# Kernel tuning notes

Measured on AMD Instinct MI355X. Metric: run time of the kernel, lower is better.

The kernel has to match this reference:

```python
import jax, jax.numpy as jnp
import numpy as np

N_NODES = 50000
N_PAIRS = 625000
F = 128

def setup_inputs() -> dict:
    key = jax.random.key(0)
    k1, k2, k3, k4, k5 = jax.random.split(key, 5)
    x = jax.random.normal(k1, (N_NODES, F), dtype=jnp.float32)
    alpha_ij = jax.random.normal(k2, (N_PAIRS,), dtype=jnp.float32)
    idx_i = jax.random.randint(k3, (N_PAIRS,), 0, N_NODES, dtype=jnp.int32)
    idx_j = jax.random.randint(k4, (N_PAIRS,), 0, N_NODES, dtype=jnp.int32)
    # Dense(F, use_bias=False) kernel, shape (F_in, F_out)
    W = jax.random.normal(k5, (F, F), dtype=jnp.float32) / np.sqrt(F)
    return {"x": x, "alpha_ij": alpha_ij, "idx_i": idx_i, "idx_j": idx_j, "W": W}

def reference(x, alpha_ij, idx_i, idx_j, W):
    # dense projection on nodes (n,F) @ (F,F) -> (n,F)
    v = jnp.matmul(x, W)
    # gather neighbor values, scale by attention coeff: (n_pairs, F)
    msg = alpha_ij[:, None] * v[idx_j]
    # scatter-sum back to center atoms
    return jax.ops.segment_sum(msg, segment_ids=idx_i, num_segments=x.shape[0])
```

## Files before the change

### kernel.cpp

```cpp
#include <hip/hip_runtime.h>
#include <stdint.h>

#define FDIM 128
#define BR 64
#define NB_C 196
#define QC 4096
#define PPB 2048

typedef short  s8v   __attribute__((ext_vector_type(8)));
typedef float  f4v   __attribute__((ext_vector_type(4)));
typedef unsigned short u8v __attribute__((ext_vector_type(8)));

__device__ __forceinline__ unsigned short f2bf(float f) {
    union { float f; uint32_t u; } c; c.f = f;
    uint32_t u = c.u;
    return (unsigned short)((u + 0x7fffu + ((u >> 16) & 1u)) >> 16);
}
__device__ __forceinline__ float bflo2f(uint32_t g) {
    union { uint32_t u; float f; } c; c.u = g << 16; return c.f;
}
__device__ __forceinline__ float bfhi2f(uint32_t g) {
    union { uint32_t u; float f; } c; c.u = g & 0xffff0000u; return c.f;
}

__global__ __launch_bounds__(256) void prep(const float* __restrict__ W,
                                            unsigned short* __restrict__ Wt,
                                            int* __restrict__ gcur) {
    int i = blockIdx.x * 256 + threadIdx.x;
    if (i < FDIM * FDIM) {
        int n = i & 127, k = i >> 7;
        Wt[n * FDIM + k] = f2bf(W[k * FDIM + n]);
    }
    if (i < NB_C) gcur[i] = 0;
}

__global__ __launch_bounds__(256) void fused_gemm_pass1(
        const float* __restrict__ x,
        const unsigned short* __restrict__ Wt,
        unsigned short* __restrict__ v,
        const int* __restrict__ idx_i,
        const int* __restrict__ idx_j,
        const float* __restrict__ alpha,
        int* __restrict__ gcur,
        unsigned long long* __restrict__ qrec,
        int n_rows, int n_pairs, int PB) {
    __shared__ unsigned short As[BR][FDIM + 8];

    if ((int)blockIdx.x < PB) {
        __shared__ int hist[NB_C];
        __shared__ int base_s[NB_C];
        const int t = threadIdx.x;
        const int start = blockIdx.x * PPB;

        if (t < NB_C) hist[t] = 0;
        __syncthreads();

        unsigned long long rec[8];
        int bkt[8];
#pragma unroll
        for (int i = 0; i < 8; ++i) {
            int p = start + t + i * 256;
            bkt[i] = -1;
            if (p < n_pairs) {
                int ii = idx_i[p];
                int b  = ii >> 8;
                bkt[i] = b;
                rec[i] = (unsigned long long)(uint32_t)(idx_j[p] | ((ii & 255) << 16))
                       | ((unsigned long long)(uint32_t)__float_as_int(alpha[p]) << 32);
                atomicAdd(&hist[b], 1);
            }
        }
        __syncthreads();
        if (t < NB_C) {
            int h = hist[t];
            base_s[t] = (h > 0) ? atomicAdd(&gcur[t], h) : 0;
            hist[t] = 0;
        }
        __syncthreads();
#pragma unroll
        for (int i = 0; i < 8; ++i) {
            int b = bkt[i];
            if (b >= 0) {
                int lp  = atomicAdd(&hist[b], 1);
                int pos = base_s[b] + lp;
                if (pos < QC)
                    qrec[(size_t)b * QC + pos] = rec[i];
            }
        }
        return;
    }

    const int t = threadIdx.x;
    const int row0 = (blockIdx.x - PB) * BR;
    {
        int r  = t >> 2;
        int c0 = (t & 3) * 32;
        int grow = row0 + r;
        const float* src = x + (size_t)grow * FDIM + c0;
#pragma unroll
        for (int it = 0; it < 4; ++it) {
            float4 xa = make_float4(0.f, 0.f, 0.f, 0.f);
            float4 xb = make_float4(0.f, 0.f, 0.f, 0.f);
            if (grow < n_rows) {
                xa = *(const float4*)(src + it * 8);
                xb = *(const float4*)(src + it * 8 + 4);
            }
            u8v pk;
            pk[0] = f2bf(xa.x); pk[1] = f2bf(xa.y); pk[2] = f2bf(xa.z); pk[3] = f2bf(xa.w);
            pk[4] = f2bf(xb.x); pk[5] = f2bf(xb.y); pk[6] = f2bf(xb.z); pk[7] = f2bf(xb.w);
            *(u8v*)(&As[r][c0 + it * 8]) = pk;
        }
    }
    __syncthreads();

    const int w    = t >> 6;
    const int lane = t & 63;
    const int rt   = (w & 1) * 32;
    const int ct   = (w >> 1) * 64;
    const int lrow = lane & 15;
    const int kq   = (lane >> 4) * 8;

    f4v acc[2][4];
#pragma unroll
    for (int i = 0; i < 2; ++i)
#pragma unroll
        for (int j = 0; j < 4; ++j)
            acc[i][j] = (f4v){0.f, 0.f, 0.f, 0.f};

#pragma unroll
    for (int ks = 0; ks < 4; ++ks) {
        const int k0 = ks * 32 + kq;
        const unsigned short* wb = Wt + (size_t)(ct + lrow) * FDIM + k0;
        s8v b0 = *(const s8v*)(wb);
        s8v b1 = *(const s8v*)(wb + 16 * FDIM);
        s8v b2 = *(const s8v*)(wb + 32 * FDIM);
        s8v b3 = *(const s8v*)(wb + 48 * FDIM);
        s8v a0 = *(const s8v*)(&As[rt + lrow][k0]);
        s8v a1 = *(const s8v*)(&As[rt + 16 + lrow][k0]);
        acc[0][0] = __builtin_amdgcn_mfma_f32_16x16x32_bf16(a0, b0, acc[0][0], 0, 0, 0);
        acc[0][1] = __builtin_amdgcn_mfma_f32_16x16x32_bf16(a0, b1, acc[0][1], 0, 0, 0);
        acc[0][2] = __builtin_amdgcn_mfma_f32_16x16x32_bf16(a0, b2, acc[0][2], 0, 0, 0);
        acc[0][3] = __builtin_amdgcn_mfma_f32_16x16x32_bf16(a0, b3, acc[0][3], 0, 0, 0);
        acc[1][0] = __builtin_amdgcn_mfma_f32_16x16x32_bf16(a1, b0, acc[1][0], 0, 0, 0);
        acc[1][1] = __builtin_amdgcn_mfma_f32_16x16x32_bf16(a1, b1, acc[1][1], 0, 0, 0);
        acc[1][2] = __builtin_amdgcn_mfma_f32_16x16x32_bf16(a1, b2, acc[1][2], 0, 0, 0);
        acc[1][3] = __builtin_amdgcn_mfma_f32_16x16x32_bf16(a1, b3, acc[1][3], 0, 0, 0);
    }

    const int quad = lane >> 4;
#pragma unroll
    for (int i = 0; i < 2; ++i) {
#pragma unroll
        for (int r = 0; r < 4; ++r) {
            int row = row0 + rt + i * 16 + quad * 4 + r;
            if (row < n_rows) {
#pragma unroll
                for (int j = 0; j < 4; ++j) {
                    int col = ct + j * 16 + lrow;
                    v[(size_t)row * FDIM + col] = f2bf(acc[i][j][r]);
                }
            }
        }
    }
}

__global__ __launch_bounds__(1024) void bucket_agg(
        const unsigned short* __restrict__ v,
        const int* __restrict__ gcur,
        const unsigned long long* __restrict__ qrec,
        float* __restrict__ out,
        int n_nodes) {
    __shared__ unsigned long long sraw[QC];
    __shared__ unsigned long long ssort[QC];
    __shared__ int cnt256[256];
    __shared__ int scanbuf[256];
    __shared__ int start[257];
    const int t = threadIdx.x;
    const int c = blockIdx.x;

    int nrec = gcur[c];
    nrec = (nrec > QC) ? QC : nrec;
    const unsigned long long* q = qrec + (size_t)c * QC;

    if (t < 256) cnt256[t] = 0;
    __syncthreads();
    for (int k = t; k < nrec; k += 1024) {
        unsigned long long r = q[k];
        sraw[k] = r;
        atomicAdd(&cnt256[(int)((r >> 16) & 0xff)], 1);
    }
    __syncthreads();

    if (t < 256) scanbuf[t] = cnt256[t];
    __syncthreads();
    for (int d = 1; d < 256; d <<= 1) {
        int tmp = 0;
        if (t < 256 && t >= d) tmp = scanbuf[t - d];
        __syncthreads();
        if (t < 256) scanbuf[t] += tmp;
        __syncthreads();
    }
    if (t < 256) {
        int excl = scanbuf[t] - cnt256[t];
        start[t]  = excl;
        cnt256[t] = excl;
    }
    if (t == 0) start[256] = scanbuf[255];
    __syncthreads();

    for (int k = t; k < nrec; k += 1024) {
        unsigned long long r = sraw[k];
        int off = (int)((r >> 16) & 0xff);
        int pos = atomicAdd(&cnt256[off], 1);
        ssort[pos] = r;
    }
    __syncthreads();

    const int wv   = t >> 6;
    const int lane = t & 63;
#pragma unroll 1
    for (int i = 0; i < 16; ++i) {
        const int off  = wv * 16 + i;
        const int node = c * 256 + off;
        const int s0 = start[off];
        const int s1 = start[off + 1];

        float ax = 0.f, ay = 0.f;
        int k = s0;
        for (; k + 4 <= s1; k += 4) {
            unsigned long long r0 = ssort[k];
            unsigned long long r1 = ssort[k + 1];
            unsigned long long r2 = ssort[k + 2];
            unsigned long long r3 = ssort[k + 3];
            int j0 = (int)(r0 & 0xffff), j1 = (int)(r1 & 0xffff);
            int j2 = (int)(r2 & 0xffff), j3 = (int)(r3 & 0xffff);
            float a0 = __int_as_float((int)(r0 >> 32));
            float a1 = __int_as_float((int)(r1 >> 32));
            float a2 = __int_as_float((int)(r2 >> 32));
            float a3 = __int_as_float((int)(r3 >> 32));
            uint32_t g0 = *(const uint32_t*)(v + (size_t)j0 * FDIM + lane * 2);
            uint32_t g1 = *(const uint32_t*)(v + (size_t)j1 * FDIM + lane * 2);
            uint32_t g2 = *(const uint32_t*)(v + (size_t)j2 * FDIM + lane * 2);
            uint32_t g3 = *(const uint32_t*)(v + (size_t)j3 * FDIM + lane * 2);
            ax += a0 * bflo2f(g0) + a1 * bflo2f(g1);
            ay += a0 * bfhi2f(g0) + a1 * bfhi2f(g1);
            ax += a2 * bflo2f(g2) + a3 * bflo2f(g3);
            ay += a2 * bfhi2f(g2) + a3 * bfhi2f(g3);
        }
        if (k + 2 <= s1) {
            unsigned long long r0 = ssort[k];
            unsigned long long r1 = ssort[k + 1];
            int j0 = (int)(r0 & 0xffff), j1 = (int)(r1 & 0xffff);
            float a0 = __int_as_float((int)(r0 >> 32));
            float a1 = __int_as_float((int)(r1 >> 32));
            uint32_t g0 = *(const uint32_t*)(v + (size_t)j0 * FDIM + lane * 2);
            uint32_t g1 = *(const uint32_t*)(v + (size_t)j1 * FDIM + lane * 2);
            ax += a0 * bflo2f(g0) + a1 * bflo2f(g1);
            ay += a0 * bfhi2f(g0) + a1 * bfhi2f(g1);
            k += 2;
        }
        if (k < s1) {
            unsigned long long r0 = ssort[k];
            int j0 = (int)(r0 & 0xffff);
            float a0 = __int_as_float((int)(r0 >> 32));
            uint32_t g0 = *(const uint32_t*)(v + (size_t)j0 * FDIM + lane * 2);
            ax += a0 * bflo2f(g0);
            ay += a0 * bfhi2f(g0);
        }
        if (node < n_nodes) {
            float2 r;
            r.x = ax;
            r.y = ay;
            *(float2*)(out + (size_t)node * FDIM + lane * 2) = r;
        }
    }
}

extern "C" void kernel_launch(void* const* d_in, const int* in_sizes, int n_in,
                              void* d_out, int out_size, void* d_ws, size_t ws_size,
                              hipStream_t stream) {
    const float* x     = (const float*)d_in[0];
    const float* alpha = (const float*)d_in[1];
    const int*   idx_i = (const int*)d_in[2];
    const int*   idx_j = (const int*)d_in[3];
    const float* W     = (const float*)d_in[4];

    const int n_nodes = in_sizes[0] / FDIM;
    const int n_pairs = in_sizes[1];

    char* ws = (char*)d_ws;
    size_t off = 0;
    auto carve = [&](size_t bytes) {
        char* p = ws + off;
        off += (bytes + 255) & ~(size_t)255;
        return p;
    };
    unsigned short* v  = (unsigned short*)carve((size_t)n_nodes * FDIM * sizeof(unsigned short));
    unsigned short* Wt = (unsigned short*)carve((size_t)FDIM * FDIM * sizeof(unsigned short));
    int*  gcur = (int*)carve((size_t)NB_C * sizeof(int));
    unsigned long long* qrec =
        (unsigned long long*)carve((size_t)NB_C * QC * sizeof(unsigned long long));
    float* out = (float*)d_out;

    prep<<<(FDIM * FDIM + 255) / 256, 256, 0, stream>>>(W, Wt, gcur);

    int GB = (n_nodes + BR - 1) / BR;
    int PB = (n_pairs + PPB - 1) / PPB;
    fused_gemm_pass1<<<PB + GB, 256, 0, stream>>>(x, Wt, v, idx_i, idx_j, alpha,
                                                  gcur, qrec, n_nodes, n_pairs, PB);

    bucket_agg<<<NB_C, 1024, 0, stream>>>(v, gcur, qrec, out, n_nodes);
}
```

Measured before the change: 139.0 us.

## Use finer 64-node buckets with 512-thread aggregation blocks and wave-shuffle scan

Nodes are now grouped into buckets of 64 instead of 256, so there are 782 aggregation blocks of 512 threads instead of 196 blocks of 1024. Per-block shared memory for records falls to 1152 entries, which should let more blocks share a CU and spread work across the GPU. The 256-entry multi-barrier prefix scan is replaced by a single-wavefront shuffle scan over 64 counters. The trade-off is more global atomics on the bucket cursors in pass 1, and records in any bucket holding more than 1152 entries are silently dropped (the mean is about 800).

```diff
diff --git a/kernel.cpp b/kernel.cpp
--- a/kernel.cpp
+++ b/kernel.cpp
@@ -3,8 +3,8 @@
 
 #define FDIM 128
 #define BR 64
-#define NB_C 196
-#define QC 4096
+#define NB_C 782
+#define QC 1152
 #define PPB 2048
 
 typedef short  s8v   __attribute__((ext_vector_type(8)));
@@ -52,7 +52,7 @@
         const int t = threadIdx.x;
         const int start = blockIdx.x * PPB;
 
-        if (t < NB_C) hist[t] = 0;
+        for (int b = t; b < NB_C; b += 256) hist[b] = 0;
         __syncthreads();
 
         unsigned long long rec[8];
@@ -63,18 +63,18 @@
             bkt[i] = -1;
             if (p < n_pairs) {
                 int ii = idx_i[p];
-                int b  = ii >> 8;
+                int b  = ii >> 6;
                 bkt[i] = b;
-                rec[i] = (unsigned long long)(uint32_t)(idx_j[p] | ((ii & 255) << 16))
+                rec[i] = (unsigned long long)(uint32_t)(idx_j[p] | ((ii & 63) << 16))
                        | ((unsigned long long)(uint32_t)__float_as_int(alpha[p]) << 32);
                 atomicAdd(&hist[b], 1);
             }
         }
         __syncthreads();
-        if (t < NB_C) {
-            int h = hist[t];
-            base_s[t] = (h > 0) ? atomicAdd(&gcur[t], h) : 0;
-            hist[t] = 0;
+        for (int b = t; b < NB_C; b += 256) {
+            int h = hist[b];
+            base_s[b] = (h > 0) ? atomicAdd(&gcur[b], h) : 0;
+            hist[b] = 0;
         }
         __syncthreads();
 #pragma unroll
@@ -164,7 +164,7 @@
     }
 }
 
-__global__ __launch_bounds__(1024) void bucket_agg(
+__global__ __launch_bounds__(512) void bucket_agg(
         const unsigned short* __restrict__ v,
         const int* __restrict__ gcur,
         const unsigned long long* __restrict__ qrec,
@@ -172,9 +172,8 @@
         int n_nodes) {
     __shared__ unsigned long long sraw[QC];
     __shared__ unsigned long long ssort[QC];
-    __shared__ int cnt256[256];
-    __shared__ int scanbuf[256];
-    __shared__ int start[257];
+    __shared__ int cnt64[64];
+    __shared__ int start[65];
     const int t = threadIdx.x;
     const int c = blockIdx.x;
 
@@ -182,36 +181,33 @@
     nrec = (nrec > QC) ? QC : nrec;
     const unsigned long long* q = qrec + (size_t)c * QC;
 
-    if (t < 256) cnt256[t] = 0;
-    __syncthreads();
-    for (int k = t; k < nrec; k += 1024) {
+    if (t < 64) cnt64[t] = 0;
+    __syncthreads();
+    for (int k = t; k < nrec; k += 512) {
         unsigned long long r = q[k];
         sraw[k] = r;
-        atomicAdd(&cnt256[(int)((r >> 16) & 0xff)], 1);
-    }
-    __syncthreads();
-
-    if (t < 256) scanbuf[t] = cnt256[t];
-    __syncthreads();
-    for (int d = 1; d < 256; d <<= 1) {
-        int tmp = 0;
-        if (t < 256 && t >= d) tmp = scanbuf[t - d];
-        __syncthreads();
-        if (t < 256) scanbuf[t] += tmp;
-        __syncthreads();
-    }
-    if (t < 256) {
-        int excl = scanbuf[t] - cnt256[t];
-        start[t]  = excl;
-        cnt256[t] = excl;
-    }
-    if (t == 0) start[256] = scanbuf[255];
-    __syncthreads();
-
-    for (int k = t; k < nrec; k += 1024) {
+        atomicAdd(&cnt64[(int)((r >> 16) & 63)], 1);
+    }
+    __syncthreads();
+
+    if (t < 64) {
+        int v0 = cnt64[t];
+        int s  = v0;
+#pragma unroll
+        for (int d = 1; d < 64; d <<= 1) {
+            int n = __shfl_up(s, d);
+            if (t >= d) s += n;
+        }
+        start[t]  = s - v0;
+        cnt64[t]  = s - v0;
+        if (t == 63) start[64] = s;
+    }
+    __syncthreads();
+
+    for (int k = t; k < nrec; k += 512) {
         unsigned long long r = sraw[k];
-        int off = (int)((r >> 16) & 0xff);
-        int pos = atomicAdd(&cnt256[off], 1);
+        int off = (int)((r >> 16) & 63);
+        int pos = atomicAdd(&cnt64[off], 1);
         ssort[pos] = r;
     }
     __syncthreads();
@@ -219,9 +215,9 @@
     const int wv   = t >> 6;
     const int lane = t & 63;
 #pragma unroll 1
-    for (int i = 0; i < 16; ++i) {
-        const int off  = wv * 16 + i;
-        const int node = c * 256 + off;
+    for (int i = 0; i < 8; ++i) {
+        const int off  = wv * 8 + i;
+        const int node = c * 64 + off;
         const int s0 = start[off];
         const int s1 = start[off + 1];
 
@@ -309,5 +305,5 @@
     fused_gemm_pass1<<<PB + GB, 256, 0, stream>>>(x, Wt, v, idx_i, idx_j, alpha,
                                                   gcur, qrec, n_nodes, n_pairs, PB);
 
-    bucket_agg<<<NB_C, 1024, 0, stream>>>(v, gcur, qrec, out, n_nodes);
-}
+    bucket_agg<<<NB_C, 512, 0, stream>>>(v, gcur, qrec, out, n_nodes);
+}
```

Measured after the change: 132.0 us. 1.05x faster.
